# Kernel optimization log

Hardware: AMD Instinct MI355X
Metric: run time of the kernel (lower is better)

Reference implementation:

```python
import jax, jax.numpy as jnp
import numpy as np

FILL = -1024.0


def setup_inputs() -> dict:
    key = jax.random.key(0)
    ks = jax.random.split(key, 8)
    B, Q, K, D, KD, VD = 4, 4096, 4096, 512, 64, 64
    s = 0.02  # small init scale for numeric sanity
    return {
        "x": jax.random.normal(ks[0], (B, Q, D), dtype=jnp.float32),
        "buffer": jax.random.normal(ks[1], (B, K, D), dtype=jnp.float32),
        "mask": jax.random.randint(ks[2], (B, Q, K), 0, 2) > 0,
        "Wq": jax.random.normal(ks[3], (KD, D), dtype=jnp.float32) * s,
        "bq": jnp.zeros((KD,), dtype=jnp.float32),
        "Wk": jax.random.normal(ks[4], (KD, D), dtype=jnp.float32) * s,
        "bk": jnp.zeros((KD,), dtype=jnp.float32),
        "Wv": jax.random.normal(ks[5], (VD, D), dtype=jnp.float32) * s,
        "bv": jnp.zeros((VD,), dtype=jnp.float32),
    }


def reference(x, buffer, mask, Wq, bq, Wk, bk, Wv, bv):
    key_dim = Wq.shape[0]
    query = x @ Wq.T + bq          # [B, Q, KD]
    keys = buffer @ Wk.T + bk      # [B, K, KD]
    vals = buffer @ Wv.T + bv      # [B, K, VD]
    logits = jnp.einsum('bqd,bkd->bqk', query, keys) / np.sqrt(key_dim).astype(np.float32)
    logits = jnp.where(mask, logits, FILL)
    # stable softmax (same math as exp(x - max) / sum)
    probs = jax.nn.softmax(logits, axis=-1)
    read = jnp.einsum('bqk,bkd->bqd', probs, vals)  # [B, Q, VD]
    return read
```

## Files before the change

### kernel.cpp

```cpp
#include <hip/hip_runtime.h>
#include <hip/hip_bf16.h>

typedef float f32x4 __attribute__((ext_vector_type(4)));
typedef __bf16 bf16x8 __attribute__((ext_vector_type(8)));
typedef unsigned long long u64;
typedef u64 u64x2 __attribute__((ext_vector_type(2)));

#define NB 4
#define NQ 4096
#define NK 4096
#define DIM 512
#define KD 64
#define PKW 128
#define NG64 (1 << 20)
#define PACK_BLOCKS 2048
#define PACK_WAVES (PACK_BLOCKS * 4)

__global__ __launch_bounds__(256, 8) void pack_kernel(
        const int* __restrict__ mask, unsigned* __restrict__ pk) {
    const int tid = threadIdx.x;
    const int w = tid >> 6, l = tid & 63;
    const int wid = blockIdx.x * 4 + w;
    u64* pk64 = (u64*)pk;
#pragma unroll 1
    for (int g0 = wid * 8; g0 < NG64; g0 += PACK_WAVES * 8) {
        const int* mb = mask + (long)g0 * 64 + l;
        int m[8];
#pragma unroll
        for (int j = 0; j < 8; j++) m[j] = mb[j * 64];
        u64 bb[8];
#pragma unroll
        for (int j = 0; j < 8; j++) bb[j] = __ballot(m[j] != 0);
        if (l == 0) {
#pragma unroll
            for (int j = 0; j < 4; j++) {
                u64x2 v = {bb[2 * j], bb[2 * j + 1]};
                *(u64x2*)(pk64 + g0 + 2 * j) = v;
            }
        }
    }
}

__device__ inline bf16x8 load_cvt8(const float* __restrict__ p) {
    float4 f0 = *(const float4*)p;
    float4 f1 = *(const float4*)(p + 4);
    bf16x8 r;
    r[0] = (__bf16)f0.x; r[1] = (__bf16)f0.y; r[2] = (__bf16)f0.z; r[3] = (__bf16)f0.w;
    r[4] = (__bf16)f1.x; r[5] = (__bf16)f1.y; r[6] = (__bf16)f1.z; r[7] = (__bf16)f1.w;
    return r;
}

__global__ __launch_bounds__(256, 4) void proj_kernel(
        const float* __restrict__ x, const float* __restrict__ buf,
        const float* __restrict__ Wq, const float* __restrict__ bq,
        const float* __restrict__ Wk, const float* __restrict__ bk,
        const float* __restrict__ Wv, const float* __restrict__ bv,
        __bf16* __restrict__ Qb, __bf16* __restrict__ Kb, __bf16* __restrict__ Vt) {
    __shared__ __align__(16) float ps[4][32][66];

    const int tid = threadIdx.x;
    const int w = tid >> 6, l = tid & 63;
    const int lr = l & 15, lk = l >> 4;
    const int rg = w >> 1, kh = w & 1;
    const bool is_q = blockIdx.x < 512;
    const int blk = is_q ? blockIdx.x : blockIdx.x - 512;
    const long rowbase = (long)blk * 32 + rg * 16;
    const int kbase = kh * 256;

    if (is_q) {
        f32x4 acc[4] = {};
#pragma unroll 4
        for (int kk = 0; kk < 256; kk += 32) {
            bf16x8 a = load_cvt8(x + (rowbase + lr) * DIM + kbase + kk + lk * 8);
#pragma unroll
            for (int nb = 0; nb < 4; nb++) {
                bf16x8 bw = load_cvt8(Wq + (long)(nb * 16 + lr) * DIM + kbase + kk + lk * 8);
                acc[nb] = __builtin_amdgcn_mfma_f32_16x16x32_bf16(a, bw, acc[nb], 0, 0, 0);
            }
        }
#pragma unroll
        for (int nb = 0; nb < 4; nb++)
#pragma unroll
            for (int i = 0; i < 4; i++)
                ps[kh * 2][rg * 16 + lk * 4 + i][nb * 16 + lr] = acc[nb][i];
        __syncthreads();
        for (int e = tid; e < 2048; e += 256) {
            int row = e >> 6, col = e & 63;
            float v = (ps[0][row][col] + ps[2][row][col] + bq[col]) * 0.125f;
            Qb[((long)blk * 32 + row) * KD + col] = (__bf16)v;
        }
    } else {
        f32x4 acck[4] = {}, accv[4] = {};
#pragma unroll 4
        for (int kk = 0; kk < 256; kk += 32) {
            bf16x8 a = load_cvt8(buf + (rowbase + lr) * DIM + kbase + kk + lk * 8);
#pragma unroll
            for (int nb = 0; nb < 4; nb++) {
                bf16x8 bwk = load_cvt8(Wk + (long)(nb * 16 + lr) * DIM + kbase + kk + lk * 8);
                bf16x8 bwv = load_cvt8(Wv + (long)(nb * 16 + lr) * DIM + kbase + kk + lk * 8);
                acck[nb] = __builtin_amdgcn_mfma_f32_16x16x32_bf16(a, bwk, acck[nb], 0, 0, 0);
                accv[nb] = __builtin_amdgcn_mfma_f32_16x16x32_bf16(a, bwv, accv[nb], 0, 0, 0);
            }
        }
#pragma unroll
        for (int nb = 0; nb < 4; nb++)
#pragma unroll
            for (int i = 0; i < 4; i++) {
                ps[kh * 2 + 0][rg * 16 + lk * 4 + i][nb * 16 + lr] = acck[nb][i];
                ps[kh * 2 + 1][rg * 16 + lk * 4 + i][nb * 16 + lr] = accv[nb][i];
            }
        __syncthreads();
        for (int e = tid; e < 2048; e += 256) {
            int row = e >> 6, col = e & 63;
            float v = ps[0][row][col] + ps[2][row][col] + bk[col];
            Kb[((long)blk * 32 + row) * KD + col] = (__bf16)v;
        }
        for (int e = tid; e < 2048; e += 256) {
            int row = e & 31, col = e >> 5;
            float v = ps[1][row][col] + ps[3][row][col] + bv[col];
            long grow = (long)blk * 32 + row;
            int b = (int)(grow >> 12), kidx = (int)(grow & 4095);
            Vt[((long)b * KD + col) * NK + kidx] = (__bf16)v;
        }
    }
}

__global__ __launch_bounds__(512, 4) void attn_kernel(
        const __bf16* __restrict__ Qb, const __bf16* __restrict__ Kb,
        const __bf16* __restrict__ Vt, const unsigned* __restrict__ pk,
        float* __restrict__ out) {
    __shared__ __align__(16) char smem[36864];

    const int tid = threadIdx.x;
    const int w = tid >> 6, l = tid & 63;
    const int lr = l & 15, lk = l >> 4;
    const int b = blockIdx.x >> 8;
    const int q0 = (blockIdx.x & 255) * 16;
    const int k0 = w * 512;

    const __bf16* Qp = Qb + ((long)b * NQ + q0) * KD;
    const __bf16* Kp = Kb + (long)b * NK * KD;
    const __bf16* Vp = Vt + (long)b * KD * NK;
    const unsigned* mp = pk + ((long)b * NQ + q0) * PKW;

    __bf16 (*pl0)[72] = (__bf16(*)[72])(smem + w * 4608);
    __bf16 (*pl1)[72] = (__bf16(*)[72])(smem + w * 4608 + 2304);

    bf16x8 qa[2];
#pragma unroll
    for (int ks = 0; ks < 2; ks++)
        qa[ks] = *(const bf16x8*)(Qp + (long)lr * KD + ks * 32 + lk * 8);

    f32x4 o[4] = {};
    float l_i[4] = {0.f, 0.f, 0.f, 0.f};

    auto tile = [&](int kt, __bf16 (*pl)[72]) {
        unsigned mw0[4], mw1[4];
#pragma unroll
        for (int i = 0; i < 4; i++) {
            uint2 mwv = *(const uint2*)(mp + (long)(lk * 4 + i) * PKW + (kt >> 5));
            mw0[i] = mwv.x; mw1[i] = mwv.y;
        }
        f32x4 s[4] = {};
#pragma unroll
        for (int ks = 0; ks < 2; ks++)
#pragma unroll
            for (int nb = 0; nb < 4; nb++) {
                bf16x8 kb = *(const bf16x8*)(Kp + (long)(kt + nb * 16 + lr) * KD + ks * 32 + lk * 8);
                s[nb] = __builtin_amdgcn_mfma_f32_16x16x32_bf16(qa[ks], kb, s[nb], 0, 0, 0);
            }
#pragma unroll
        for (int nb = 0; nb < 4; nb++) {
            const unsigned bit = (unsigned)((nb * 16 + lr) & 31);
#pragma unroll
            for (int i = 0; i < 4; i++) {
                unsigned wv = (nb < 2) ? mw0[i] : mw1[i];
                float e = __expf(s[nb][i]);
                float p = ((wv >> bit) & 1u) ? e : 0.0f;
                __bf16 pb = (__bf16)p;
                pl[lk * 4 + i][nb * 16 + lr] = pb;
                l_i[i] += (float)pb;
            }
        }
#pragma unroll
        for (int ks = 0; ks < 2; ks++) {
            bf16x8 pa = *(const bf16x8*)&pl[lr][ks * 32 + lk * 8];
#pragma unroll
            for (int nb = 0; nb < 4; nb++) {
                bf16x8 vb = *(const bf16x8*)(Vp + (long)(nb * 16 + lr) * NK + kt + ks * 32 + lk * 8);
                o[nb] = __builtin_amdgcn_mfma_f32_16x16x32_bf16(pa, vb, o[nb], 0, 0, 0);
            }
        }
    };

#pragma unroll 1
    for (int kt = k0; kt < k0 + 512; kt += 128) {
        tile(kt, pl0);
        tile(kt + 64, pl1);
    }

#pragma unroll
    for (int i = 0; i < 4; i++) {
        float v = l_i[i];
        v += __shfl_xor(v, 1);
        v += __shfl_xor(v, 2);
        v += __shfl_xor(v, 4);
        v += __shfl_xor(v, 8);
        l_i[i] = v;
    }

    __syncthreads();
    float* o_s = (float*)smem;
    float* ml  = (float*)(smem + 8 * 16 * 66 * 4);
#pragma unroll
    for (int nb = 0; nb < 4; nb++)
#pragma unroll
        for (int i = 0; i < 4; i++)
            o_s[(w * 16 + lk * 4 + i) * 66 + nb * 16 + lr] = o[nb][i];
    if (lr == 0) {
#pragma unroll
        for (int i = 0; i < 4; i++)
            ml[w * 16 + lk * 4 + i] = l_i[i];
    }
    __syncthreads();
    for (int e = tid; e < 1024; e += 512) {
        int row = e >> 6, col = e & 63;
        float L = 0.f, O = 0.f;
#pragma unroll
        for (int ww = 0; ww < 8; ww++) {
            L += ml[ww * 16 + row];
            O += o_s[(ww * 16 + row) * 66 + col];
        }
        out[((long)b * NQ + q0 + row) * KD + col] = O / L;
    }
}

extern "C" void kernel_launch(void* const* d_in, const int* in_sizes, int n_in,
                              void* d_out, int out_size, void* d_ws, size_t ws_size,
                              hipStream_t stream) {
    const float* x      = (const float*)d_in[0];
    const float* buffer = (const float*)d_in[1];
    const int*   mask   = (const int*)d_in[2];
    const float* Wq     = (const float*)d_in[3];
    const float* bq     = (const float*)d_in[4];
    const float* Wk     = (const float*)d_in[5];
    const float* bk     = (const float*)d_in[6];
    const float* Wv     = (const float*)d_in[7];
    const float* bv     = (const float*)d_in[8];
    float* out = (float*)d_out;

    unsigned* pk = (unsigned*)d_ws;
    __bf16* Qb = (__bf16*)((char*)d_ws + (size_t)NB * NQ * PKW * 4);
    __bf16* Kb = Qb + (size_t)NB * NQ * KD;
    __bf16* Vt = Kb + (size_t)NB * NK * KD;

    pack_kernel<<<dim3(PACK_BLOCKS), dim3(256), 0, stream>>>(mask, pk);
    proj_kernel<<<dim3(1024), dim3(256), 0, stream>>>(x, buffer, Wq, bq, Wk, bk, Wv, bv, Qb, Kb, Vt);
    attn_kernel<<<dim3(NB * (NQ / 16)), dim3(512), 0, stream>>>(Qb, Kb, Vt, pk, out);
}
```

Before: 266.3 us.

## Pack mask with 16-byte loads into interleaved bit layout for attention

The pack kernel now reads the int mask with int4 vector loads and emits four ballots per load, so the bitmask comes out in an interleaved layout where each 256-key chunk is stored as four 64-bit words. The attention kernel reads one 64-bit word per row per tile and shifts by a lane-dependent amount to get its per-lane mask bits. This cuts load instructions in the bandwidth-bound pack pass and simplifies the mask extraction in the softmax loop. It also changes the packed layout contract between the two kernels, which must stay consistent.

```diff
diff --git a/kernel.cpp b/kernel.cpp
--- a/kernel.cpp
+++ b/kernel.cpp
@@ -11,31 +11,37 @@
 #define NK 4096
 #define DIM 512
 #define KD 64
-#define PKW 128
-#define NG64 (1 << 20)
+#define NCH (NB * NQ * (NK / 256))
 #define PACK_BLOCKS 2048
 #define PACK_WAVES (PACK_BLOCKS * 4)
 
 __global__ __launch_bounds__(256, 8) void pack_kernel(
-        const int* __restrict__ mask, unsigned* __restrict__ pk) {
+        const int* __restrict__ mask, u64* __restrict__ pk64) {
     const int tid = threadIdx.x;
     const int w = tid >> 6, l = tid & 63;
     const int wid = blockIdx.x * 4 + w;
-    u64* pk64 = (u64*)pk;
+    const long ch0 = (long)wid * 32;
 #pragma unroll 1
-    for (int g0 = wid * 8; g0 < NG64; g0 += PACK_WAVES * 8) {
-        const int* mb = mask + (long)g0 * 64 + l;
-        int m[8];
-#pragma unroll
-        for (int j = 0; j < 8; j++) m[j] = mb[j * 64];
-        u64 bb[8];
-#pragma unroll
-        for (int j = 0; j < 8; j++) bb[j] = __ballot(m[j] != 0);
+    for (int it = 0; it < 4; ++it) {
+        const long ch = ch0 + it * 8;
+        const int4* mb = (const int4*)(mask + ch * 256) + l;
+        int4 v[8];
+#pragma unroll
+        for (int j = 0; j < 8; j++) v[j] = mb[j * 64];
+        u64 bb[32];
+#pragma unroll
+        for (int j = 0; j < 8; j++) {
+            bb[j * 4 + 0] = __ballot(v[j].x != 0);
+            bb[j * 4 + 1] = __ballot(v[j].y != 0);
+            bb[j * 4 + 2] = __ballot(v[j].z != 0);
+            bb[j * 4 + 3] = __ballot(v[j].w != 0);
+        }
         if (l == 0) {
-#pragma unroll
-            for (int j = 0; j < 4; j++) {
-                u64x2 v = {bb[2 * j], bb[2 * j + 1]};
-                *(u64x2*)(pk64 + g0 + 2 * j) = v;
+            u64* dst = pk64 + ch * 4;
+#pragma unroll
+            for (int j = 0; j < 16; j++) {
+                u64x2 t = {bb[2 * j], bb[2 * j + 1]};
+                *(u64x2*)(dst + 2 * j) = t;
             }
         }
     }
@@ -127,7 +133,7 @@
 
 __global__ __launch_bounds__(512, 4) void attn_kernel(
         const __bf16* __restrict__ Qb, const __bf16* __restrict__ Kb,
-        const __bf16* __restrict__ Vt, const unsigned* __restrict__ pk,
+        const __bf16* __restrict__ Vt, const u64* __restrict__ pk64,
         float* __restrict__ out) {
     __shared__ __align__(16) char smem[36864];
 
@@ -141,7 +147,7 @@
     const __bf16* Qp = Qb + ((long)b * NQ + q0) * KD;
     const __bf16* Kp = Kb + (long)b * NK * KD;
     const __bf16* Vp = Vt + (long)b * KD * NK;
-    const unsigned* mp = pk + ((long)b * NQ + q0) * PKW;
+    const u64* mp64 = pk64 + ((long)b * NQ + q0 + lk * 4) * 64 + (lr & 3);
 
     __bf16 (*pl0)[72] = (__bf16(*)[72])(smem + w * 4608);
     __bf16 (*pl1)[72] = (__bf16(*)[72])(smem + w * 4608 + 2304);
@@ -155,12 +161,11 @@
     float l_i[4] = {0.f, 0.f, 0.f, 0.f};
 
     auto tile = [&](int kt, __bf16 (*pl)[72]) {
-        unsigned mw0[4], mw1[4];
-#pragma unroll
-        for (int i = 0; i < 4; i++) {
-            uint2 mwv = *(const uint2*)(mp + (long)(lk * 4 + i) * PKW + (kt >> 5));
-            mw0[i] = mwv.x; mw1[i] = mwv.y;
-        }
+        const int sh = ((kt & 255) >> 2) + (lr >> 2);
+        unsigned mt[4];
+#pragma unroll
+        for (int i = 0; i < 4; i++)
+            mt[i] = (unsigned)(mp64[(long)i * 64 + (kt >> 8) * 4] >> sh);
         f32x4 s[4] = {};
 #pragma unroll
         for (int ks = 0; ks < 2; ks++)
@@ -170,18 +175,15 @@
                 s[nb] = __builtin_amdgcn_mfma_f32_16x16x32_bf16(qa[ks], kb, s[nb], 0, 0, 0);
             }
 #pragma unroll
-        for (int nb = 0; nb < 4; nb++) {
-            const unsigned bit = (unsigned)((nb * 16 + lr) & 31);
+        for (int nb = 0; nb < 4; nb++)
 #pragma unroll
             for (int i = 0; i < 4; i++) {
-                unsigned wv = (nb < 2) ? mw0[i] : mw1[i];
                 float e = __expf(s[nb][i]);
-                float p = ((wv >> bit) & 1u) ? e : 0.0f;
+                float p = ((mt[i] >> (nb * 4)) & 1u) ? e : 0.0f;
                 __bf16 pb = (__bf16)p;
                 pl[lk * 4 + i][nb * 16 + lr] = pb;
                 l_i[i] += (float)pb;
             }
-        }
 #pragma unroll
         for (int ks = 0; ks < 2; ks++) {
             bf16x8 pa = *(const bf16x8*)&pl[lr][ks * 32 + lk * 8];
@@ -249,12 +251,12 @@
     const float* bv     = (const float*)d_in[8];
     float* out = (float*)d_out;
 
-    unsigned* pk = (unsigned*)d_ws;
-    __bf16* Qb = (__bf16*)((char*)d_ws + (size_t)NB * NQ * PKW * 4);
+    u64* pk64 = (u64*)d_ws;
+    __bf16* Qb = (__bf16*)((char*)d_ws + (size_t)NCH * 4 * 8);
     __bf16* Kb = Qb + (size_t)NB * NQ * KD;
     __bf16* Vt = Kb + (size_t)NB * NK * KD;
 
-    pack_kernel<<<dim3(PACK_BLOCKS), dim3(256), 0, stream>>>(mask, pk);
+    pack_kernel<<<dim3(PACK_BLOCKS), dim3(256), 0, stream>>>(mask, pk64);
     proj_kernel<<<dim3(1024), dim3(256), 0, stream>>>(x, buffer, Wq, bq, Wk, bk, Wv, bv, Qb, Kb, Vt);
-    attn_kernel<<<dim3(NB * (NQ / 16)), dim3(512), 0, stream>>>(Qb, Kb, Vt, pk, out);
-}
+    attn_kernel<<<dim3(NB * (NQ / 16)), dim3(512), 0, stream>>>(Qb, Kb, Vt, pk64, out);
+}
```

Result: no change. 268.6 us (+0.9%).
